# Kernel tuning notes

Measured on AMD Instinct MI355X. Metric: run time of the kernel, lower is better.

The kernel has to match this reference:

```python
import jax, jax.numpy as jnp
import numpy as np

# dims from source: seq_len=784, d_in=2, d_hidden=512, d_out=2, n_layers=3; batch bumped 32->64
T, BS, D_IN, D_H, D_OUT, N_LAYERS = 784, 64, 2, 512, 2, 3


def _glorot(k, shape):
    fan_in, fan_out = shape[-2], shape[-1]
    std = jnp.sqrt(2.0 / (fan_in + fan_out)).astype(jnp.float32)
    return jax.random.normal(k, shape, jnp.float32) * std


def setup_inputs() -> dict:
    key = jax.random.key(0)
    ks = jax.random.split(key, 8)
    x = jax.random.normal(ks[0], (T, BS, D_IN), jnp.float32)
    W0 = _glorot(ks[1], (D_IN, D_H))
    b0 = jnp.zeros((D_H,), jnp.float32)
    # stable_init: uniform in [0.999, 1.001), one diagonal 'a' per layer
    A = jax.random.uniform(ks[2], (N_LAYERS, D_H), jnp.float32, 0.999, 1.001)
    B = _glorot(ks[3], (N_LAYERS, D_H, D_H))  # per-layer input matrix b
    C = _glorot(ks[4], (N_LAYERS, D_H, D_H))  # per-layer output matrix c
    Wf = _glorot(ks[5], (D_H, D_OUT))
    bf = jnp.zeros((D_OUT,), jnp.float32)
    return {"x": x, "W0": W0, "b0": b0, "A": A, "B": B, "C": C, "Wf": Wf, "bf": bf}


def _rnn_layer(x, a, b, c):
    # x: [T, BS, D], diagonal linear recurrence h_t = h_{t-1} * a + x_t @ b; y_t = h_t @ c
    u = jnp.einsum('tbi,ih->tbh', x, b)  # batched GEMM outside the scan

    def step(h, u_t):
        h = h * a + u_t
        return h, h

    h0 = jnp.zeros(u.shape[1:], u.dtype)  # [BS, D_H]
    _, hs = jax.lax.scan(step, h0, u)     # hs: [T, BS, D_H]
    return jnp.einsum('tbh,ho->tbo', hs, c)


def reference(x, W0, b0, A, B, C, Wf, bf):
    # initial Dense + relu
    h = jax.nn.relu(x @ W0 + b0)
    # stacked unidirectional RNN layers, relu after each
    for l in range(A.shape[0]):
        h = jax.nn.relu(_rnn_layer(h, A[l], B[l], C[l]))
    # final Dense (no residual)
    return h @ Wf + bf
```

## Files before the change

kernel.cpp:

```cpp
#include <hip/hip_runtime.h>
#include <hip/hip_bf16.h>

typedef _Float16 f16;
typedef f16 f16x8 __attribute__((ext_vector_type(8)));
typedef float f32x4 __attribute__((ext_vector_type(4)));

#define T_LEN 784
#define BATCH 64
#define DH 512
#define NCH (BATCH*DH)
#define M_ROWS (T_LEN*BATCH)
#define NCHUNK 16
#define CLEN 49

#define ACT_SCALE (1.0f/256.0f)
#define ACT_INV   256.0f

#define GLL16(g, s)                                                             \
    __builtin_amdgcn_global_load_lds(                                           \
        (const __attribute__((address_space(1))) void*)(g),                     \
        (__attribute__((address_space(3))) void*)(s), 16, 0, 0)

#define VMCNT(n) asm volatile("s_waitcnt vmcnt(" #n ")" ::: "memory")

__global__ void prep_weights(const float* __restrict__ B, const float* __restrict__ C,
                             f16* __restrict__ Bt, f16* __restrict__ Ct) {
    __shared__ float tile[32][33];
    int z = blockIdx.z;
    const float* src = (z < 3) ? (B + (size_t)z * DH * DH) : (C + (size_t)(z - 3) * DH * DH);
    f16* dst = (z < 3) ? (Bt + (size_t)z * DH * DH) : (Ct + (size_t)(z - 3) * DH * DH);
    int tx = threadIdx.x, ty = threadIdx.y;
    int nb = blockIdx.x * 32, kb = blockIdx.y * 32;
#pragma unroll
    for (int i = 0; i < 4; i++) {
        int k = ty + i * 8;
        tile[k][tx] = src[(size_t)(kb + k) * DH + nb + tx];
    }
    __syncthreads();
#pragma unroll
    for (int i = 0; i < 4; i++) {
        int n = ty + i * 8;
        dst[(size_t)(nb + n) * DH + kb + tx] = (f16)tile[tx][n];
    }
}

__global__ void dense0_kernel(const float* __restrict__ x, const float* __restrict__ W0,
                              const float* __restrict__ b0, f16* __restrict__ H) {
    int tid = blockIdx.x * 256 + threadIdx.x;
    int m = tid >> 6;
    int hb = (tid & 63) * 8;
    float x0 = x[(size_t)m * 2], x1 = x[(size_t)m * 2 + 1];
    f32x4 wa0 = *(const f32x4*)(W0 + hb);
    f32x4 wa1 = *(const f32x4*)(W0 + hb + 4);
    f32x4 wb0 = *(const f32x4*)(W0 + DH + hb);
    f32x4 wb1 = *(const f32x4*)(W0 + DH + hb + 4);
    f32x4 c0 = *(const f32x4*)(b0 + hb);
    f32x4 c1 = *(const f32x4*)(b0 + hb + 4);
    f16x8 o;
#pragma unroll
    for (int j = 0; j < 4; j++) {
        float v = fmaxf(fmaf(x0, wa0[j], fmaf(x1, wb0[j], c0[j])), 0.f) * ACT_SCALE;
        o[j] = (f16)v;
    }
#pragma unroll
    for (int j = 0; j < 4; j++) {
        float v = fmaxf(fmaf(x0, wa1[j], fmaf(x1, wb1[j], c1[j])), 0.f) * ACT_SCALE;
        o[4 + j] = (f16)v;
    }
    *(f16x8*)(H + (size_t)m * DH + hb) = o;
}

template <int RELU>
__global__ __launch_bounds__(256) void gemm_k(const f16* __restrict__ A,
                                              const f16* __restrict__ Bt,
                                              f16* __restrict__ Out) {
    __shared__ __align__(16) f16 As[3][128 * 32];
    __shared__ __align__(16) f16 Bs[3][128 * 32];
    const int tid = threadIdx.x;
    const int lane = tid & 63;
    const int wave = tid >> 6;
    const int wr = wave >> 1, wc = wave & 1;
    const size_t mb = (size_t)blockIdx.x * 128;
    const int nb = blockIdx.y * 128;

    const int rl = lane >> 2, sl = lane & 3;
    const int ssl = sl ^ ((rl >> 1) & 3);
    const int rowS0 = wave * 16 + rl;
    const int rowS1 = 64 + wave * 16 + rl;
    const f16* gA0 = A + (mb + rowS0) * DH + ssl * 8;
    const f16* gA1 = A + (mb + rowS1) * DH + ssl * 8;
    const f16* gB0 = Bt + (size_t)(nb + rowS0) * DH + ssl * 8;
    const f16* gB1 = Bt + (size_t)(nb + rowS1) * DH + ssl * 8;
    const int ldsOff0 = (wave * 16) * 32;
    const int ldsOff1 = (64 + wave * 16) * 32;

    const int rA = lane & 15, kq = lane >> 4;
    const int fsl = kq ^ ((rA >> 1) & 3);
    int offA[4], offB[4];
#pragma unroll
    for (int i = 0; i < 4; i++) offA[i] = (wr * 64 + i * 16 + rA) * 32 + fsl * 8;
#pragma unroll
    for (int j = 0; j < 4; j++) offB[j] = (wc * 64 + j * 16 + rA) * 32 + fsl * 8;

    f32x4 acc[4][4] = {};

#define STAGE(b, kt)                        \
    do {                                    \
        GLL16(gA0 + (kt), &As[b][ldsOff0]); \
        GLL16(gA1 + (kt), &As[b][ldsOff1]); \
        GLL16(gB0 + (kt), &Bs[b][ldsOff0]); \
        GLL16(gB1 + (kt), &Bs[b][ldsOff1]); \
    } while (0)

#define COMPUTE(b)                                                                              \
    do {                                                                                        \
        f16x8 af[4], bg[4];                                                                     \
        _Pragma("unroll") for (int i = 0; i < 4; i++) af[i] = *(const f16x8*)&As[b][offA[i]];   \
        _Pragma("unroll") for (int j = 0; j < 4; j++) bg[j] = *(const f16x8*)&Bs[b][offB[j]];   \
        _Pragma("unroll") for (int i = 0; i < 4; i++)                                           \
        _Pragma("unroll") for (int j = 0; j < 4; j++)                                           \
            acc[i][j] = __builtin_amdgcn_mfma_f32_16x16x32_f16(af[i], bg[j], acc[i][j], 0, 0, 0); \
    } while (0)

    STAGE(0, 0);
    STAGE(1, 32);

#pragma unroll
    for (int t = 0; t < 15; ++t) {
        VMCNT(4);
        __builtin_amdgcn_s_barrier();
        if (t < 14) STAGE((t + 2) % 3, (t + 2) * 32);
        COMPUTE(t % 3);
    }
    VMCNT(0);
    __builtin_amdgcn_s_barrier();
    COMPUTE(0);
#undef STAGE
#undef COMPUTE

    const int crow = (lane >> 4) * 4;
    const int ccol = lane & 15;
#pragma unroll
    for (int i = 0; i < 4; i++)
#pragma unroll
        for (int j = 0; j < 4; j++) {
#pragma unroll
            for (int r = 0; r < 4; r++) {
                size_t row = mb + wr * 64 + i * 16 + crow + r;
                int col = nb + wc * 64 + j * 16 + ccol;
                float v = acc[i][j][r];
                if (RELU) v = fmaxf(v, 0.f);
                Out[row * DH + col] = (f16)v;
            }
        }
}

__global__ void scan_pass1(const f16* __restrict__ U, const float* __restrict__ Al,
                           float* __restrict__ finals) {
    int tid = blockIdx.x * 256 + threadIdx.x;
    int ch = tid & (NCH - 1);
    int c = tid >> 15;
    float a = Al[ch & (DH - 1)];
    const f16* p = U + (size_t)(c * CLEN) * NCH + ch;
    float h = 0.f;
#pragma unroll
    for (int i = 0; i < CLEN; i++) h = fmaf(h, a, (float)p[(size_t)i * NCH]);
    finals[(size_t)c * NCH + ch] = h;
}

__global__ void scan_pass3(f16* __restrict__ U, const float* __restrict__ Al,
                           const float* __restrict__ finals) {
    int tid = blockIdx.x * 256 + threadIdx.x;
    int ch = tid & (NCH - 1);
    int c = tid >> 15;
    float a = Al[ch & (DH - 1)];
    float a49 = 1.f;
#pragma unroll
    for (int i = 0; i < CLEN; i++) a49 *= a;
    float carry = 0.f;
    for (int cc = 0; cc < c; cc++)
        carry = fmaf(carry, a49, finals[(size_t)cc * NCH + ch]);
    f16* p = U + (size_t)(c * CLEN) * NCH + ch;
    float h = carry;
#pragma unroll
    for (int i = 0; i < CLEN; i++) {
        h = fmaf(h, a, (float)p[(size_t)i * NCH]);
        p[(size_t)i * NCH] = (f16)h;
    }
}

__global__ void final_dense(const f16* __restrict__ H, const float* __restrict__ Wf,
                            const float* __restrict__ bf_, float* __restrict__ out) {
    __shared__ float WfS[DH * 2];
    for (int i = threadIdx.x; i < DH * 2; i += 256) WfS[i] = Wf[i];
    __syncthreads();
    int wave = threadIdx.x >> 6, lane = threadIdx.x & 63;
    size_t m = (size_t)blockIdx.x * 4 + wave;
    f16x8 v = *(const f16x8*)(H + m * DH + lane * 8);
    float d0 = 0.f, d1 = 0.f;
#pragma unroll
    for (int j = 0; j < 8; j++) {
        float hv = (float)v[j];
        int h = lane * 8 + j;
        d0 = fmaf(hv, WfS[h * 2], d0);
        d1 = fmaf(hv, WfS[h * 2 + 1], d1);
    }
#pragma unroll
    for (int off = 32; off; off >>= 1) {
        d0 += __shfl_down(d0, off);
        d1 += __shfl_down(d1, off);
    }
    if (lane == 0) {
        out[m * 2] = fmaf(d0, ACT_INV, bf_[0]);
        out[m * 2 + 1] = fmaf(d1, ACT_INV, bf_[1]);
    }
}

extern "C" void kernel_launch(void* const* d_in, const int* in_sizes, int n_in,
                              void* d_out, int out_size, void* d_ws, size_t ws_size,
                              hipStream_t stream) {
    (void)in_sizes; (void)n_in; (void)out_size; (void)ws_size;
    const float* x   = (const float*)d_in[0];
    const float* W0  = (const float*)d_in[1];
    const float* b0  = (const float*)d_in[2];
    const float* A   = (const float*)d_in[3];
    const float* Bw  = (const float*)d_in[4];
    const float* Cw  = (const float*)d_in[5];
    const float* Wf  = (const float*)d_in[6];
    const float* bfv = (const float*)d_in[7];
    float* out = (float*)d_out;

    char* ws = (char*)d_ws;
    size_t off = 0;
    auto alloc = [&](size_t bytes) {
        void* p = ws + off;
        off += (bytes + 255) & ~(size_t)255;
        return p;
    };
    f16* Bt = (f16*)alloc((size_t)3 * DH * DH * 2);
    f16* Ct = (f16*)alloc((size_t)3 * DH * DH * 2);
    f16* P  = (f16*)alloc((size_t)M_ROWS * DH * 2);
    f16* Q  = (f16*)alloc((size_t)M_ROWS * DH * 2);
    float* finals  = (float*)alloc((size_t)NCH * NCHUNK * 4);

    dim3 b256(256);
    prep_weights<<<dim3(16, 16, 6), dim3(32, 8), 0, stream>>>(Bw, Cw, Bt, Ct);
    dense0_kernel<<<M_ROWS * 64 / 256, b256, 0, stream>>>(x, W0, b0, P);
    for (int l = 0; l < 3; l++) {
        const float* Al = A + l * DH;
        gemm_k<0><<<dim3(M_ROWS / 128, 4), b256, 0, stream>>>(P, Bt + (size_t)l * DH * DH, Q);
        scan_pass1<<<NCH * NCHUNK / 256, b256, 0, stream>>>(Q, Al, finals);
        scan_pass3<<<NCH * NCHUNK / 256, b256, 0, stream>>>(Q, Al, finals);
        gemm_k<1><<<dim3(M_ROWS / 128, 4), b256, 0, stream>>>(Q, Ct + (size_t)l * DH * DH, P);
    }
    final_dense<<<M_ROWS / 4, b256, 0, stream>>>(P, Wf, bfv, out);
}
```

Before: 360.6 us.

## Replace 128x128 GEMM with 8-wave 256x256 tile and 4-stage half-tile pipeline

```diff
diff --git a/kernel.cpp b/kernel.cpp
--- a/kernel.cpp
+++ b/kernel.cpp
@@ -22,6 +22,7 @@
         (__attribute__((address_space(3))) void*)(s), 16, 0, 0)
 
 #define VMCNT(n) asm volatile("s_waitcnt vmcnt(" #n ")" ::: "memory")
+#define SBAR()   asm volatile("s_barrier" ::: "memory")
 
 __global__ void prep_weights(const float* __restrict__ B, const float* __restrict__ C,
                              f16* __restrict__ Bt, f16* __restrict__ Ct) {
@@ -71,88 +72,113 @@
 }
 
 template <int RELU>
-__global__ __launch_bounds__(256) void gemm_k(const f16* __restrict__ A,
-                                              const f16* __restrict__ Bt,
-                                              f16* __restrict__ Out) {
-    __shared__ __align__(16) f16 As[3][128 * 32];
-    __shared__ __align__(16) f16 Bs[3][128 * 32];
+__global__ __launch_bounds__(512, 2) void gemm8(const f16* __restrict__ A,
+                                                const f16* __restrict__ Bt,
+                                                f16* __restrict__ Out) {
+    __shared__ __align__(16) f16 As[4][128 * 64];
+    __shared__ __align__(16) f16 Bs[4][128 * 64];
     const int tid = threadIdx.x;
     const int lane = tid & 63;
     const int wave = tid >> 6;
-    const int wr = wave >> 1, wc = wave & 1;
-    const size_t mb = (size_t)blockIdx.x * 128;
-    const int nb = blockIdx.y * 128;
-
-    const int rl = lane >> 2, sl = lane & 3;
-    const int ssl = sl ^ ((rl >> 1) & 3);
-    const int rowS0 = wave * 16 + rl;
-    const int rowS1 = 64 + wave * 16 + rl;
-    const f16* gA0 = A + (mb + rowS0) * DH + ssl * 8;
-    const f16* gA1 = A + (mb + rowS1) * DH + ssl * 8;
-    const f16* gB0 = Bt + (size_t)(nb + rowS0) * DH + ssl * 8;
-    const f16* gB1 = Bt + (size_t)(nb + rowS1) * DH + ssl * 8;
-    const int ldsOff0 = (wave * 16) * 32;
-    const int ldsOff1 = (64 + wave * 16) * 32;
+    const int wm = wave >> 2;
+    const int wn = wave & 3;
+    const size_t mb = (size_t)blockIdx.x * 256;
+    const int nb = blockIdx.y * 256;
+
+    const int srw = tid >> 3;
+    const int ss = (tid & 7) ^ (srw & 7);
+    const int ldsR0 = (wave * 8) * 64;
+    const int ldsR1 = (64 + wave * 8) * 64;
+
+#define SA(H)                                                                                  \
+    do {                                                                                       \
+        GLL16(A + (mb + ((H) & 1) * 128 + srw) * DH + ((H) >> 1) * 64 + ss * 8,                \
+              &As[(H) & 3][ldsR0]);                                                            \
+        GLL16(A + (mb + ((H) & 1) * 128 + 64 + srw) * DH + ((H) >> 1) * 64 + ss * 8,           \
+              &As[(H) & 3][ldsR1]);                                                            \
+    } while (0)
+#define SB(H)                                                                                  \
+    do {                                                                                       \
+        GLL16(Bt + ((size_t)nb + ((H) & 1) * 128 + srw) * DH + ((H) >> 1) * 64 + ss * 8,       \
+              &Bs[(H) & 3][ldsR0]);                                                            \
+        GLL16(Bt + ((size_t)nb + ((H) & 1) * 128 + 64 + srw) * DH + ((H) >> 1) * 64 + ss * 8,  \
+              &Bs[(H) & 3][ldsR1]);                                                            \
+    } while (0)
 
     const int rA = lane & 15, kq = lane >> 4;
-    const int fsl = kq ^ ((rA >> 1) & 3);
-    int offA[4], offB[4];
-#pragma unroll
-    for (int i = 0; i < 4; i++) offA[i] = (wr * 64 + i * 16 + rA) * 32 + fsl * 8;
-#pragma unroll
-    for (int j = 0; j < 4; j++) offB[j] = (wc * 64 + j * 16 + rA) * 32 + fsl * 8;
-
-    f32x4 acc[4][4] = {};
-
-#define STAGE(b, kt)                        \
-    do {                                    \
-        GLL16(gA0 + (kt), &As[b][ldsOff0]); \
-        GLL16(gA1 + (kt), &As[b][ldsOff1]); \
-        GLL16(gB0 + (kt), &Bs[b][ldsOff0]); \
-        GLL16(gB1 + (kt), &Bs[b][ldsOff1]); \
-    } while (0)
-
-#define COMPUTE(b)                                                                              \
-    do {                                                                                        \
-        f16x8 af[4], bg[4];                                                                     \
-        _Pragma("unroll") for (int i = 0; i < 4; i++) af[i] = *(const f16x8*)&As[b][offA[i]];   \
-        _Pragma("unroll") for (int j = 0; j < 4; j++) bg[j] = *(const f16x8*)&Bs[b][offB[j]];   \
-        _Pragma("unroll") for (int i = 0; i < 4; i++)                                           \
-        _Pragma("unroll") for (int j = 0; j < 4; j++)                                           \
-            acc[i][j] = __builtin_amdgcn_mfma_f32_16x16x32_f16(af[i], bg[j], acc[i][j], 0, 0, 0); \
-    } while (0)
-
-    STAGE(0, 0);
-    STAGE(1, 32);
-
-#pragma unroll
-    for (int t = 0; t < 15; ++t) {
-        VMCNT(4);
-        __builtin_amdgcn_s_barrier();
-        if (t < 14) STAGE((t + 2) % 3, (t + 2) * 32);
-        COMPUTE(t % 3);
-    }
-    VMCNT(0);
-    __builtin_amdgcn_s_barrier();
-    COMPUTE(0);
-#undef STAGE
-#undef COMPUTE
+    int aoff[2][2], boff[4][2];
+#pragma unroll
+    for (int fr = 0; fr < 2; fr++)
+#pragma unroll
+        for (int ks = 0; ks < 2; ks++)
+            aoff[fr][ks] = (fr * 16 + rA) * 64 + ((ks * 4 + kq) ^ (rA & 7)) * 8;
+#pragma unroll
+    for (int fc = 0; fc < 4; fc++)
+#pragma unroll
+        for (int ks = 0; ks < 2; ks++)
+            boff[fc][ks] = ((wn & 1) * 64 + fc * 16 + rA) * 64 + ((ks * 4 + kq) ^ (rA & 7)) * 8;
+
+    f32x4 acc[4][2][4] = {};
+
+    SA(0); SA(1); SB(0); SB(1); SA(2);
+
+#pragma unroll
+    for (int kt = 0; kt < 8; ++kt) {
+        f16x8 bg[4][2];
+#pragma unroll
+        for (int q = 0; q < 4; ++q) {
+            if (q == 0) {
+                if (kt < 7) { VMCNT(2); } else { VMCNT(0); }
+                SBAR();
+                if (kt <= 6) { SA(2 * kt + 3); SB(2 * kt + 2); }
+                const f16* pb = &Bs[(2 * kt + (wn >> 1)) & 3][0];
+#pragma unroll
+                for (int fc = 0; fc < 4; fc++)
+#pragma unroll
+                    for (int ks = 0; ks < 2; ks++)
+                        bg[fc][ks] = *(const f16x8*)(pb + boff[fc][ks]);
+            }
+            if (q == 1 && kt <= 6) SB(2 * kt + 3);
+            if (q == 2 && kt <= 5) SA(2 * kt + 4);
+            const f16* pa = &As[(2 * kt + (q >> 1)) & 3][((q & 1) * 64 + wm * 32) * 64];
+            f16x8 af[2][2];
+#pragma unroll
+            for (int fr = 0; fr < 2; fr++)
+#pragma unroll
+                for (int ks = 0; ks < 2; ks++)
+                    af[fr][ks] = *(const f16x8*)(pa + aoff[fr][ks]);
+            __builtin_amdgcn_s_setprio(1);
+#pragma unroll
+            for (int fr = 0; fr < 2; fr++)
+#pragma unroll
+                for (int fc = 0; fc < 4; fc++)
+#pragma unroll
+                    for (int ks = 0; ks < 2; ks++)
+                        acc[q][fr][fc] = __builtin_amdgcn_mfma_f32_16x16x32_f16(
+                            af[fr][ks], bg[fc][ks], acc[q][fr][fc], 0, 0, 0);
+            __builtin_amdgcn_s_setprio(0);
+            if (q < 3) SBAR();
+        }
+    }
+#undef SA
+#undef SB
 
     const int crow = (lane >> 4) * 4;
     const int ccol = lane & 15;
 #pragma unroll
-    for (int i = 0; i < 4; i++)
-#pragma unroll
-        for (int j = 0; j < 4; j++) {
-#pragma unroll
-            for (int r = 0; r < 4; r++) {
-                size_t row = mb + wr * 64 + i * 16 + crow + r;
-                int col = nb + wc * 64 + j * 16 + ccol;
-                float v = acc[i][j][r];
-                if (RELU) v = fmaxf(v, 0.f);
-                Out[row * DH + col] = (f16)v;
-            }
-        }
+    for (int q = 0; q < 4; ++q)
+#pragma unroll
+        for (int fr = 0; fr < 2; ++fr)
+#pragma unroll
+            for (int fc = 0; fc < 4; ++fc)
+#pragma unroll
+                for (int r = 0; r < 4; ++r) {
+                    size_t row = mb + q * 64 + wm * 32 + fr * 16 + crow + r;
+                    int col = nb + wn * 64 + fc * 16 + ccol;
+                    float v = acc[q][fr][fc][r];
+                    if (RELU) v = fmaxf(v, 0.f);
+                    Out[row * DH + col] = (f16)v;
+                }
 }
 
 __global__ void scan_pass1(const f16* __restrict__ U, const float* __restrict__ Al,
@@ -244,14 +270,16 @@
     float* finals  = (float*)alloc((size_t)NCH * NCHUNK * 4);
 
     dim3 b256(256);
+    dim3 b512(512);
+    dim3 ggrid(M_ROWS / 256, 2);
     prep_weights<<<dim3(16, 16, 6), dim3(32, 8), 0, stream>>>(Bw, Cw, Bt, Ct);
     dense0_kernel<<<M_ROWS * 64 / 256, b256, 0, stream>>>(x, W0, b0, P);
     for (int l = 0; l < 3; l++) {
         const float* Al = A + l * DH;
-        gemm_k<0><<<dim3(M_ROWS / 128, 4), b256, 0, stream>>>(P, Bt + (size_t)l * DH * DH, Q);
+        gemm8<0><<<ggrid, b512, 0, stream>>>(P, Bt + (size_t)l * DH * DH, Q);
         scan_pass1<<<NCH * NCHUNK / 256, b256, 0, stream>>>(Q, Al, finals);
         scan_pass3<<<NCH * NCHUNK / 256, b256, 0, stream>>>(Q, Al, finals);
-        gemm_k<1><<<dim3(M_ROWS / 128, 4), b256, 0, stream>>>(Q, Ct + (size_t)l * DH * DH, P);
+        gemm8<1><<<ggrid, b512, 0, stream>>>(Q, Ct + (size_t)l * DH * DH, P);
     }
     final_dense<<<M_ROWS / 4, b256, 0, stream>>>(P, Wf, bfv, out);
 }
```

Result: no change. 365.3 us (+1.3%).

## Make GEMM persistent over 7 M-tiles per block with continuous pipeline

Applied to the files above, without the earlier changes.

```diff
diff --git a/kernel.cpp b/kernel.cpp
--- a/kernel.cpp
+++ b/kernel.cpp
@@ -2,6 +2,7 @@
 #include <hip/hip_bf16.h>
 
 typedef _Float16 f16;
+typedef f16 f16x4 __attribute__((ext_vector_type(4)));
 typedef f16 f16x8 __attribute__((ext_vector_type(8)));
 typedef float f32x4 __attribute__((ext_vector_type(4)));
 
@@ -71,7 +72,7 @@
 }
 
 template <int RELU>
-__global__ __launch_bounds__(256) void gemm_k(const f16* __restrict__ A,
+__global__ __launch_bounds__(256) void gemm_p(const f16* __restrict__ A,
                                               const f16* __restrict__ Bt,
                                               f16* __restrict__ Out) {
     __shared__ __align__(16) f16 As[3][128 * 32];
@@ -80,15 +81,14 @@
     const int lane = tid & 63;
     const int wave = tid >> 6;
     const int wr = wave >> 1, wc = wave & 1;
-    const size_t mb = (size_t)blockIdx.x * 128;
-    const int nb = blockIdx.y * 128;
+    const int blk = blockIdx.x;
+    const int nb = (blk / 56) * 128;
+    const int r0 = (blk % 56) * 7;
 
     const int rl = lane >> 2, sl = lane & 3;
     const int ssl = sl ^ ((rl >> 1) & 3);
     const int rowS0 = wave * 16 + rl;
     const int rowS1 = 64 + wave * 16 + rl;
-    const f16* gA0 = A + (mb + rowS0) * DH + ssl * 8;
-    const f16* gA1 = A + (mb + rowS1) * DH + ssl * 8;
     const f16* gB0 = Bt + (size_t)(nb + rowS0) * DH + ssl * 8;
     const f16* gB1 = Bt + (size_t)(nb + rowS1) * DH + ssl * 8;
     const int ldsOff0 = (wave * 16) * 32;
@@ -104,12 +104,16 @@
 
     f32x4 acc[4][4] = {};
 
-#define STAGE(b, kt)                        \
-    do {                                    \
-        GLL16(gA0 + (kt), &As[b][ldsOff0]); \
-        GLL16(gA1 + (kt), &As[b][ldsOff1]); \
-        GLL16(gB0 + (kt), &Bs[b][ldsOff0]); \
-        GLL16(gB1 + (kt), &Bs[b][ldsOff1]); \
+#define STAGE_S(s2, slot)                                                          \
+    do {                                                                           \
+        int ti_ = (s2) >> 4;                                                       \
+        int kt_ = ((s2) & 15) * 32;                                                \
+        const f16* a0 = A + ((size_t)((r0 + ti_) * 128 + rowS0)) * DH + kt_ + ssl * 8; \
+        const f16* a1 = A + ((size_t)((r0 + ti_) * 128 + rowS1)) * DH + kt_ + ssl * 8; \
+        GLL16(a0, &As[slot][ldsOff0]);                                             \
+        GLL16(a1, &As[slot][ldsOff1]);                                             \
+        GLL16(gB0 + kt_, &Bs[slot][ldsOff0]);                                      \
+        GLL16(gB1 + kt_, &Bs[slot][ldsOff1]);                                      \
     } while (0)
 
 #define COMPUTE(b)                                                                              \
@@ -119,40 +123,48 @@
         _Pragma("unroll") for (int j = 0; j < 4; j++) bg[j] = *(const f16x8*)&Bs[b][offB[j]];   \
         _Pragma("unroll") for (int i = 0; i < 4; i++)                                           \
         _Pragma("unroll") for (int j = 0; j < 4; j++)                                           \
-            acc[i][j] = __builtin_amdgcn_mfma_f32_16x16x32_f16(af[i], bg[j], acc[i][j], 0, 0, 0); \
+            acc[i][j] = __builtin_amdgcn_mfma_f32_16x16x32_f16(bg[j], af[i], acc[i][j], 0, 0, 0); \
     } while (0)
 
-    STAGE(0, 0);
-    STAGE(1, 32);
-
-#pragma unroll
-    for (int t = 0; t < 15; ++t) {
-        VMCNT(4);
+    STAGE_S(0, 0);
+    STAGE_S(1, 1);
+
+    const int erow = lane & 15;
+    const int ecq = (lane >> 4) * 4;
+    int cb = 0, sb = 2;
+    for (int s = 0; s < 112; ++s) {
+        if (s < 110) { VMCNT(4); } else { VMCNT(0); }
         __builtin_amdgcn_s_barrier();
-        if (t < 14) STAGE((t + 2) % 3, (t + 2) * 32);
-        COMPUTE(t % 3);
-    }
-    VMCNT(0);
-    __builtin_amdgcn_s_barrier();
-    COMPUTE(0);
-#undef STAGE
+        if (s < 110) STAGE_S(s + 2, sb);
+        COMPUTE(cb);
+        if ((s & 15) == 15) {
+            size_t mb = (size_t)(r0 + (s >> 4)) * 128;
+#pragma unroll
+            for (int i = 0; i < 4; i++) {
+                size_t row = mb + wr * 64 + i * 16 + erow;
+#pragma unroll
+                for (int j = 0; j < 4; j++) {
+                    int col = nb + wc * 64 + j * 16 + ecq;
+                    f16x4 o;
+#pragma unroll
+                    for (int r = 0; r < 4; r++) {
+                        float v = acc[i][j][r];
+                        if (RELU) v = fmaxf(v, 0.f);
+                        o[r] = (f16)v;
+                    }
+                    *(f16x4*)(Out + row * DH + col) = o;
+                }
+            }
+#pragma unroll
+            for (int i = 0; i < 4; i++)
+#pragma unroll
+                for (int j = 0; j < 4; j++) acc[i][j] = (f32x4){0.f, 0.f, 0.f, 0.f};
+        }
+        cb = (cb == 2) ? 0 : cb + 1;
+        sb = (sb == 2) ? 0 : sb + 1;
+    }
+#undef STAGE_S
 #undef COMPUTE
-
-    const int crow = (lane >> 4) * 4;
-    const int ccol = lane & 15;
-#pragma unroll
-    for (int i = 0; i < 4; i++)
-#pragma unroll
-        for (int j = 0; j < 4; j++) {
-#pragma unroll
-            for (int r = 0; r < 4; r++) {
-                size_t row = mb + wr * 64 + i * 16 + crow + r;
-                int col = nb + wc * 64 + j * 16 + ccol;
-                float v = acc[i][j][r];
-                if (RELU) v = fmaxf(v, 0.f);
-                Out[row * DH + col] = (f16)v;
-            }
-        }
 }
 
 __global__ void scan_pass1(const f16* __restrict__ U, const float* __restrict__ Al,
@@ -248,10 +260,10 @@
     dense0_kernel<<<M_ROWS * 64 / 256, b256, 0, stream>>>(x, W0, b0, P);
     for (int l = 0; l < 3; l++) {
         const float* Al = A + l * DH;
-        gemm_k<0><<<dim3(M_ROWS / 128, 4), b256, 0, stream>>>(P, Bt + (size_t)l * DH * DH, Q);
+        gemm_p<0><<<dim3(224), b256, 0, stream>>>(P, Bt + (size_t)l * DH * DH, Q);
         scan_pass1<<<NCH * NCHUNK / 256, b256, 0, stream>>>(Q, Al, finals);
         scan_pass3<<<NCH * NCHUNK / 256, b256, 0, stream>>>(Q, Al, finals);
-        gemm_k<1><<<dim3(M_ROWS / 128, 4), b256, 0, stream>>>(Q, Ct + (size_t)l * DH * DH, P);
+        gemm_p<1><<<dim3(224), b256, 0, stream>>>(Q, Ct + (size_t)l * DH * DH, P);
     }
     final_dense<<<M_ROWS / 4, b256, 0, stream>>>(P, Wf, bfv, out);
 }
```

Result: slower. 765.1 us (+112.2%).
